# Kernel tuning notes

Measured on AMD Instinct MI355X. Metric: run time of the kernel, lower is better.

The kernel has to match this reference:

```python
import jax, jax.numpy as jnp
import numpy as np

BATCH, NUM_BSS, NUM_USERS, M, N = 32, 8, 32, 128, 4
LAGR_ITERS = 8
PSEUDOINV_SVAL_THRESH = 1e-12


def herm(a):
    return 0.5 * (a + jnp.swapaxes(a, -1, -2).conj())


def setup_inputs() -> dict:
    key = jax.random.key(0)
    ks = jax.random.split(key, 7)
    v_re = jax.random.normal(ks[0], (BATCH, NUM_USERS, M, N), jnp.float32)
    v_im = jax.random.normal(ks[1], (BATCH, NUM_USERS, M, N), jnp.float32)
    H_re = jax.random.normal(ks[2], (NUM_BSS, NUM_USERS, N, M), jnp.float32)
    H_im = jax.random.normal(ks[3], (NUM_BSS, NUM_USERS, N, M), jnp.float32)
    noise_pow = jax.random.uniform(ks[4], (BATCH, NUM_USERS), jnp.float32, 0.05, 1.0)
    rweights = jax.random.uniform(ks[5], (BATCH, NUM_USERS), jnp.float32, 0.1, 1.0)
    bss_pow = jnp.ones((BATCH, NUM_BSS), jnp.float32)
    assign = jax.random.randint(ks[6], (NUM_USERS,), 0, NUM_BSS).astype(jnp.int32)
    return {"v_re": v_re, "v_im": v_im, "H_re": H_re, "H_im": H_im,
            "noise_pow": noise_pow, "rweights": rweights, "bss_pow": bss_pow,
            "assign": assign}


def reference(v_re, v_im, H_re, H_im, noise_pow, rweights, bss_pow, assign):
    V = v_re + 1j * v_im          # [B,K,M,N] precoders
    H = H_re + 1j * H_im          # [C,K,N,M] channel BS c -> user k
    K = V.shape[1]
    C = H.shape[0]
    Ndim = V.shape[-1]
    eyeN = jnp.eye(Ndim, dtype=V.dtype)

    # Hg[j, i] = channel from assigned-BS-of-user-j to user i
    Hg = H[assign]                                    # [K,K,N,M]
    # downlink covariance per user i: noise*I + sum_j (H[bs_j,i] V_j)(.)^H
    HV = jnp.einsum('jinm,bjmp->bijnp', Hg, V)        # [B,Ki,Kj,N,N]
    cov = jnp.einsum('bijnp,bijqp->binq', HV, HV.conj())
    cov = herm(cov + noise_pow[..., None, None] * eyeN)
    icov = herm(jnp.linalg.inv(cov))                  # [B,K,N,N]

    idx = jnp.arange(K)
    Hd = Hg[idx, idx]                                 # [K,N,M] direct channels
    HdV = jnp.einsum('knm,bkmp->bknp', Hd, V)         # [B,K,N,N]
    u = jnp.einsum('bknq,bkqp->bknp', icov, HdV)      # receive filters
    w_inv = herm(eyeN - jnp.einsum('bkqn,bkqp->bknp', u.conj(), HdV))
    w = herm(jnp.linalg.inv(w_inv))                   # MSE weights (w_poly=None)
    uwu = herm(jnp.einsum('bknp,bkpq,bkrq->bknr', u, w, u.conj()))
    # v_tilde = H_ii^H u w * rate_weight
    vt = jnp.einsum('knm,bknp,bkpq->bkmq', Hd.conj(), u, w) * rweights[..., None, None]

    # uplink covariance per BS c: sum_k rw_k * H[c,k]^H uwu_k H[c,k]
    ul = herm(jnp.einsum('cknm,bkno,ckop,bk->bcmp', H.conj(), uwu, H, rweights))

    # aux per BS: sum over assigned users of v_tilde v_tilde^H
    Q = jnp.einsum('bkmn,bkpn->bkmp', vt, vt.conj())  # [B,K,M,M]
    aux = jnp.moveaxis(
        jax.ops.segment_sum(jnp.moveaxis(Q, 1, 0), assign, num_segments=C), 0, 1)  # [B,C,M,M]

    lam, E = jnp.linalg.eigh(ul)                      # [B,C,M], [B,C,M,M]
    lam = jnp.maximum(lam, 0.0)
    c = jnp.maximum(jnp.einsum('bcmi,bcmp,bcpi->bci', E.conj(), aux, E).real, 0.0)
    c = c / bss_pow[..., None]

    # solve sum_i c_i/(lam_i+mu)^2 = 1 for mu >= 0 by bisection in [0, sqrt(sum c)]
    hi = jnp.sqrt(jnp.sum(c, -1))
    lo = jnp.zeros_like(hi)
    for _ in range(LAGR_ITERS):
        mid = 0.5 * (lo + hi)
        f = jnp.sum(c / jnp.square(lam + mid[..., None] + 1e-20), -1)
        gt = f > 1.0
        lo = jnp.where(gt, mid, lo)
        hi = jnp.where(gt, hi, mid)
    mu = jnp.maximum(0.5 * (lo + hi), 0.0)            # [B,C]

    # pseudo-inverse of loaded UL covariance via its eigendecomposition
    lam_l = lam + mu[..., None]
    lam_l = jnp.where(lam_l < PSEUDOINV_SVAL_THRESH, 1e12, lam_l)
    inv_aug = herm(jnp.einsum('bcmi,bci,bcni->bcmn', E, 1.0 / lam_l, E.conj()))

    # v update: v_k = inv_aug[assign_k] @ v_tilde_k
    v_out = jnp.einsum('bkmp,bkpn->bkmn', inv_aug[:, assign], vt)  # [B,K,M,N]
    return v_out
```

## Files before the change

kernel.cpp:

```cpp
#include <hip/hip_runtime.h>

#define B_ 32
#define C_ 8
#define K_ 32

__device__ __forceinline__ float2 cmul(float2 a, float2 b) {
  return make_float2(a.x*b.x - a.y*b.y, a.x*b.y + a.y*b.x);
}
__device__ __forceinline__ float2 cmulc(float2 a, float2 b) {
  return make_float2(a.x*b.x + a.y*b.y, a.y*b.x - a.x*b.y);
}
__device__ __forceinline__ float2 cadd(float2 a, float2 b){ return make_float2(a.x+b.x, a.y+b.y); }
__device__ __forceinline__ float2 csub(float2 a, float2 b){ return make_float2(a.x-b.x, a.y-b.y); }
__device__ __forceinline__ int SK(int r){ return r + ((r >> 3) << 1); }

__device__ void herm4_inv(float2 a[4][4], float2 out[4][4]) {
  float idg[4];
  for (int j = 0; j < 4; ++j) {
    float d = sqrtf(fmaxf(a[j][j].x, 1e-30f));
    float id = 1.f / d;
    idg[j] = id;
    a[j][j] = make_float2(d, 0.f);
    for (int r = j+1; r < 4; ++r) { a[r][j].x *= id; a[r][j].y *= id; }
    for (int c = j+1; c < 4; ++c)
      for (int r = c; r < 4; ++r)
        a[r][c] = csub(a[r][c], cmulc(a[r][j], a[c][j]));
  }
  float2 li[4][4];
  for (int j = 0; j < 4; ++j) {
    li[j][j] = make_float2(idg[j], 0.f);
    for (int r = j+1; r < 4; ++r) {
      float2 s = make_float2(0.f, 0.f);
      for (int d = j; d < r; ++d) s = cadd(s, cmul(a[r][d], li[d][j]));
      li[r][j] = make_float2(-s.x*idg[r], -s.y*idg[r]);
    }
  }
  for (int p = 0; p < 4; ++p)
    for (int q = 0; q < 4; ++q) {
      float2 s = make_float2(0.f, 0.f);
      for (int d = (p > q ? p : q); d < 4; ++d)
        s = cadd(s, cmulc(li[d][q], li[d][p]));
      out[p][q] = s;
    }
}

__global__ __launch_bounds__(512, 2) void k_fused(
    const float* __restrict__ v_re, const float* __restrict__ v_im,
    const float* __restrict__ H_re, const float* __restrict__ H_im,
    const float* __restrict__ noise_pow, const float* __restrict__ rweights,
    const float* __restrict__ bss_pow, const int* __restrict__ assign_g,
    void* __restrict__ outp, int omode)
{
  const int t = threadIdx.x;
  const int lane = t & 63, wid = t >> 6;
  const int blk = blockIdx.x;
  const int b = blk >> 3, c = blk & 7;
  const int tm = t >> 4, tp = t & 15;
  const int rbase = tm * 4, cbase = tp * 8;

  __shared__ __align__(16) float2 Arena[4160];
  __shared__ __align__(16) float2 pS[1024];
  __shared__ __align__(16) float2 dBS2[256];
  __shared__ __align__(16) float2 vS[128];
  __shared__ __align__(16) float2 wS[160];
  __shared__ __align__(16) float2 colS[160];
  __shared__ __align__(16) float2 pvS[128];
  __shared__ __align__(16) float2 tauS[128];
  __shared__ float dS[128], eS[128], cpS[128];
  __shared__ float red[8];
  __shared__ int asg[K_], ulist[K_], nc_s;

  float2* Wall = pS;
  float2* uwS  = pS + 512;
  float2* Vs   = Arena;
  float2* Tb   = Arena + 776;
  float2* covS = Arena + 1288;
  float2* HdVS = Arena + 1800;
  float2* Hs   = Arena;
  float2* Ys   = Arena + 520;
  float2* Pd   = Arena;
  float2* Bs   = Arena;

  if (t < K_) asg[t] = assign_g[t];
  if (t == 0) {
    int n2 = 0;
    for (int k = 0; k < K_; ++k) if (assign_g[k] == c) ulist[n2++] = k;
    nc_s = n2;
  }
  {
    const int k = t >> 4, n = (t >> 2) & 3, q = t & 3;
    covS[t] = make_float2((n == q) ? noise_pow[b*K_ + k] : 0.f, 0.f);
  }
  __syncthreads();
  const int nc = nc_s;
  if (nc == 0) return;
  const int cols = 4 * nc;
  const int qmax = (cols + 15) >> 4;
  const int passes = (cols + 31) >> 5;

  {
    const int pn = t >> 2;
    const int qt = t & 3;
    const int kk = pn >> 2, nn = pn & 3;
    const float2* Vq = Vs + qt*2;
    for (int j = 0; j < K_; ++j) {
      const int vb = (b*K_ + j) * 512;
      Vs[(t >> 2)*6 + (t & 3) + (t >> 7)*2] = make_float2(v_re[vb + t], v_im[vb + t]);
      __syncthreads();
      const int hb = ((asg[j]*K_ + kk)*4 + nn) * 128;
      float2 a0 = {0,0}, a1 = {0,0}, a2 = {0,0}, a3 = {0,0};
      for (int m4 = qt*32; m4 < qt*32 + 32; m4 += 4) {
        const float4 hre = *(const float4*)&H_re[hb + m4];
        const float4 him = *(const float4*)&H_im[hb + m4];
        const float hx[4] = {hre.x, hre.y, hre.z, hre.w};
        const float hy[4] = {him.x, him.y, him.z, him.w};
        #pragma unroll
        for (int i = 0; i < 4; ++i) {
          const float4 v01 = *(const float4*)&Vq[(m4 + i)*6];
          const float4 v23 = *(const float4*)&Vq[(m4 + i)*6 + 2];
          a0.x += hx[i]*v01.x - hy[i]*v01.y; a0.y += hx[i]*v01.y + hy[i]*v01.x;
          a1.x += hx[i]*v01.z - hy[i]*v01.w; a1.y += hx[i]*v01.w + hy[i]*v01.z;
          a2.x += hx[i]*v23.x - hy[i]*v23.y; a2.y += hx[i]*v23.y + hy[i]*v23.x;
          a3.x += hx[i]*v23.z - hy[i]*v23.w; a3.y += hx[i]*v23.w + hy[i]*v23.z;
        }
      }
      #pragma unroll
      for (int o = 1; o <= 2; o <<= 1) {
        a0.x += __shfl_xor(a0.x, o, 64); a0.y += __shfl_xor(a0.y, o, 64);
        a1.x += __shfl_xor(a1.x, o, 64); a1.y += __shfl_xor(a1.y, o, 64);
        a2.x += __shfl_xor(a2.x, o, 64); a2.y += __shfl_xor(a2.y, o, 64);
        a3.x += __shfl_xor(a3.x, o, 64); a3.y += __shfl_xor(a3.y, o, 64);
      }
      if (qt == 0) {
        Tb[pn*4 + 0] = a0; Tb[pn*4 + 1] = a1; Tb[pn*4 + 2] = a2; Tb[pn*4 + 3] = a3;
      }
      __syncthreads();
      {
        const int k2 = t >> 4, n2 = (t >> 2) & 3, q2 = t & 3;
        float2 acc = covS[t];
        #pragma unroll
        for (int p = 0; p < 4; ++p)
          acc = cadd(acc, cmulc(Tb[(k2*4 + n2)*4 + p], Tb[(k2*4 + q2)*4 + p]));
        covS[t] = acc;
        if (k2 == j) HdVS[k2*16 + n2*4 + q2] = Tb[(k2*4 + n2)*4 + q2];
      }
      __syncthreads();
    }
  }

  if (t < K_) {
    const int k = t;
    float2 a[4][4], ic[4][4], hv[4][4], u[4][4], wi[4][4], w[4][4], uw[4][4], W[4][4];
    const float rwk = rweights[b*K_ + k];
    for (int r = 0; r < 4; ++r)
      for (int c2 = 0; c2 < 4; ++c2) a[r][c2] = covS[k*16 + r*4 + c2];
    herm4_inv(a, ic);
    for (int r = 0; r < 4; ++r)
      for (int c2 = 0; c2 < 4; ++c2) hv[r][c2] = HdVS[k*16 + r*4 + c2];
    for (int n = 0; n < 4; ++n)
      for (int p = 0; p < 4; ++p) {
        float2 s = {0,0};
        for (int q = 0; q < 4; ++q) s = cadd(s, cmul(ic[n][q], hv[q][p]));
        u[n][p] = s;
      }
    for (int n = 0; n < 4; ++n)
      for (int p = 0; p < 4; ++p) {
        float2 s = make_float2((n == p) ? 1.f : 0.f, 0.f);
        for (int q = 0; q < 4; ++q) s = csub(s, cmulc(hv[q][p], u[q][n]));
        wi[n][p] = s;
      }
    herm4_inv(wi, w);
    for (int n = 0; n < 4; ++n)
      for (int q = 0; q < 4; ++q) {
        float2 s = {0,0};
        for (int p = 0; p < 4; ++p) s = cadd(s, cmul(u[n][p], w[p][q]));
        uw[n][q] = s;
      }
    for (int n = 0; n < 4; ++n)
      for (int r = 0; r < 4; ++r) {
        float2 s = {0,0};
        for (int q = 0; q < 4; ++q) s = cadd(s, cmulc(uw[n][q], u[r][q]));
        W[n][r] = make_float2(s.x * rwk, s.y * rwk);
      }
    for (int n = 0; n < 4; ++n)
      for (int r = n; r < 4; ++r) {
        float2 x1 = W[n][r], x2 = W[r][n];
        float2 hm = make_float2(0.5f*(x1.x + x2.x), 0.5f*(x1.y - x2.y));
        W[n][r] = hm; W[r][n] = make_float2(hm.x, -hm.y);
      }
    for (int idx = 0; idx < 16; ++idx) {
      uwS[k*16 + idx]  = uw[idx >> 2][idx & 3];
      Wall[k*16 + idx] = W[idx >> 2][idx & 3];
    }
  }
  __syncthreads();

  float2 Bv[4][8];
  #pragma unroll
  for (int j = 0; j < 4; ++j)
    #pragma unroll
    for (int q = 0; q < 8; ++q) Bv[j][q] = make_float2(0.f, 0.f);
  float trp = 0.f;
  #pragma unroll
  for (int q = 0; q < 8; ++q) {
    const int col = tp + 16*q;
    const int slot = col >> 2, qn = col & 3;
    if (slot < nc) {
      const int k = ulist[slot];
      const float rwk = rweights[b*K_ + k];
      const int hb = (c*K_ + k) * 512;
      float2 acc0 = {0,0}, acc1 = {0,0}, acc2 = {0,0}, acc3 = {0,0};
      #pragma unroll
      for (int n = 0; n < 4; ++n) {
        const float2 uwv = uwS[k*16 + n*4 + qn];
        const float4 hre = *(const float4*)&H_re[hb + n*128 + rbase];
        const float4 him = *(const float4*)&H_im[hb + n*128 + rbase];
        acc0 = cadd(acc0, cmulc(uwv, make_float2(hre.x, him.x)));
        acc1 = cadd(acc1, cmulc(uwv, make_float2(hre.y, him.y)));
        acc2 = cadd(acc2, cmulc(uwv, make_float2(hre.z, him.z)));
        acc3 = cadd(acc3, cmulc(uwv, make_float2(hre.w, him.w)));
      }
      acc0.x *= rwk; acc0.y *= rwk; acc1.x *= rwk; acc1.y *= rwk;
      acc2.x *= rwk; acc2.y *= rwk; acc3.x *= rwk; acc3.y *= rwk;
      Bv[0][q] = acc0; Bv[1][q] = acc1; Bv[2][q] = acc2; Bv[3][q] = acc3;
      trp += acc0.x*acc0.x + acc0.y*acc0.y + acc1.x*acc1.x + acc1.y*acc1.y
           + acc2.x*acc2.x + acc2.y*acc2.y + acc3.x*acc3.x + acc3.y*acc3.y;
    }
  }
  #pragma unroll
  for (int o = 32; o >= 1; o >>= 1) trp += __shfl_xor(trp, o, 64);
  if (lane == 0) red[wid] = trp;
  __syncthreads();
  const float inv_bss = 1.f / bss_pow[b*C_ + c];
  float hi = sqrtf((red[0] + red[1] + red[2] + red[3] +
                    red[4] + red[5] + red[6] + red[7]) * inv_bss);
  float lo = 0.f;

  float2 Areg[4][8];
  #pragma unroll
  for (int j = 0; j < 4; ++j)
    #pragma unroll
    for (int cc = 0; cc < 8; ++cc) Areg[j][cc] = make_float2(0.f, 0.f);
  __syncthreads();
  for (int k = 0; k < K_; ++k) {
    const int hb = (c*K_ + k) * 512;
    Hs[(t >> 7)*130 + (t & 127)] = make_float2(H_re[hb + t], H_im[hb + t]);
    __syncthreads();
    {
      const int n = t >> 7, p = t & 127;
      float2 y = {0,0};
      #pragma unroll
      for (int o = 0; o < 4; ++o) y = cadd(y, cmul(Wall[k*16 + n*4 + o], Hs[o*130 + p]));
      Ys[n*160 + p + ((p >> 3) << 1)] = y;
    }
    __syncthreads();
    #pragma unroll
    for (int n = 0; n < 4; ++n) {
      float2 h[4], y[8];
      {
        const float4 ha = *(const float4*)&Hs[n*130 + rbase];
        const float4 hc = *(const float4*)&Hs[n*130 + rbase + 2];
        h[0] = make_float2(ha.x, ha.y); h[1] = make_float2(ha.z, ha.w);
        h[2] = make_float2(hc.x, hc.y); h[3] = make_float2(hc.z, hc.w);
        const float2* yb = &Ys[n*160 + tp*10];
        #pragma unroll
        for (int a2 = 0; a2 < 8; a2 += 2) {
          const float4 y4 = *(const float4*)&yb[a2];
          y[a2] = make_float2(y4.x, y4.y); y[a2+1] = make_float2(y4.z, y4.w);
        }
      }
      #pragma unroll
      for (int j = 0; j < 4; ++j)
        #pragma unroll
        for (int cc = 0; cc < 8; ++cc) {
          Areg[j][cc].x += h[j].x*y[cc].x + h[j].y*y[cc].y;
          Areg[j][cc].y += h[j].x*y[cc].y - h[j].y*y[cc].x;
        }
    }
    __syncthreads();
  }

  if (tp == 0) {
    #pragma unroll
    for (int j = 0; j < 4; ++j) colS[SK(rbase + j)] = Areg[j][0];
  }
  __syncthreads();

  #pragma unroll 1
  for (int i = 0; i < 127; ++i) {
    float2 vr[4], vc[8], tau, sc;
    {
      const float2 x0 = colS[SK(lane)], x1 = colS[SK(lane + 64)];
      float sig = 0.f;
      if (lane >= i + 2)      sig += x0.x*x0.x + x0.y*x0.y;
      if (lane + 64 >= i + 2) sig += x1.x*x1.x + x1.y*x1.y;
      #pragma unroll
      for (int o = 32; o >= 1; o >>= 1) sig += __shfl_xor(sig, o, 64);
      const float2 al = colS[SK(i + 1)];
      float beta;
      if (sig <= 1e-30f && fabsf(al.y) <= 1e-30f) {
        beta = al.x; tau = make_float2(0.f, 0.f); sc = make_float2(0.f, 0.f);
      } else {
        const float mag = sqrtf(al.x*al.x + al.y*al.y + sig);
        beta = (al.x >= 0.f) ? -mag : mag;
        const float ib = 1.f / beta;
        tau = make_float2((beta - al.x) * ib, -al.y * ib);
        const float dx = al.x - beta, dy = al.y;
        const float dn = 1.f / (dx*dx + dy*dy);
        sc = make_float2(dx*dn, -dy*dn);
      }
      if (t == 0) { eS[i] = beta; tauS[i] = tau; }
      #pragma unroll
      for (int j = 0; j < 4; ++j) {
        const int r = rbase + j;
        const float2 x = colS[SK(r)];
        vr[j] = (r <= i) ? make_float2(0.f, 0.f)
              : (r == i + 1 ? make_float2(1.f, 0.f) : cmul(x, sc));
      }
      {
        const int cb = SK(cbase);
        const float4 c01 = *(const float4*)&colS[cb];
        const float4 c23 = *(const float4*)&colS[cb + 2];
        const float4 c45 = *(const float4*)&colS[cb + 4];
        const float4 c67 = *(const float4*)&colS[cb + 6];
        const float2 cx[8] = { make_float2(c01.x,c01.y), make_float2(c01.z,c01.w),
                               make_float2(c23.x,c23.y), make_float2(c23.z,c23.w),
                               make_float2(c45.x,c45.y), make_float2(c45.z,c45.w),
                               make_float2(c67.x,c67.y), make_float2(c67.z,c67.w) };
        #pragma unroll
        for (int cc = 0; cc < 8; ++cc) {
          const int r = cbase + cc;
          vc[cc] = (r <= i) ? make_float2(0.f, 0.f)
                 : (r == i + 1 ? make_float2(1.f, 0.f) : cmul(cx[cc], sc));
        }
      }
    }
    {
      float2 part[4];
      #pragma unroll
      for (int j = 0; j < 4; ++j) {
        float2 s = cmul(Areg[j][0], vc[0]);
        #pragma unroll
        for (int cc = 1; cc < 8; ++cc) s = cadd(s, cmul(Areg[j][cc], vc[cc]));
        part[j] = s;
      }
      #pragma unroll
      for (int o = 1; o <= 8; o <<= 1) {
        #pragma unroll
        for (int j = 0; j < 4; ++j) {
          part[j].x += __shfl_xor(part[j].x, o, 64);
          part[j].y += __shfl_xor(part[j].y, o, 64);
        }
      }
      #pragma unroll
      for (int j = 0; j < 4; ++j) if (tp == j) pvS[rbase + j] = part[j];
      #pragma unroll
      for (int q = 0; q < 8; ++q) {
        if (q >= qmax) continue;
        float2 s = {0.f, 0.f};
        #pragma unroll
        for (int j = 0; j < 4; ++j) s = cadd(s, cmulc(Bv[j][q], vr[j]));
        Pd[tm*130 + tp + 16*q] = s;
      }
    }
    __syncthreads();

    if (wid == 0) {
      float2 p0 = {0.f,0.f}, p1 = {0.f,0.f};
      if (lane > i)      p0 = cmul(tau, pvS[lane]);
      if (lane + 64 > i) p1 = cmul(tau, pvS[lane + 64]);
      float2 v0, v1;
      v0 = (lane <= i) ? make_float2(0.f,0.f)
         : (lane == i + 1 ? make_float2(1.f,0.f) : cmul(colS[SK(lane)], sc));
      { const int r1 = lane + 64;
        v1 = (r1 <= i) ? make_float2(0.f,0.f)
           : (r1 == i + 1 ? make_float2(1.f,0.f) : cmul(colS[SK(r1)], sc)); }
      float2 d0 = cadd(cmulc(p0, v0), cmulc(p1, v1));
      #pragma unroll
      for (int o = 32; o >= 1; o >>= 1) {
        d0.x += __shfl_xor(d0.x, o, 64);
        d0.y += __shfl_xor(d0.y, o, 64);
      }
      const float alr = -0.5f * (tau.x*d0.x + tau.y*d0.y);
      wS[SK(lane)]      = cadd(p0, make_float2(alr*v0.x, alr*v0.y));
      wS[SK(lane + 64)] = cadd(p1, make_float2(alr*v1.x, alr*v1.y));
    } else if (t < 320) {
      const int col = (t - 64) & 127;
      const int half = (t - 64) >> 7;
      float2 s = {0.f, 0.f};
      #pragma unroll
      for (int g = 0; g < 16; ++g) s = cadd(s, Pd[(half*16 + g)*130 + col]);
      dBS2[half*128 + col] = s;
    }
    __syncthreads();

    {
      float2 wr[4], wc[8];
      #pragma unroll
      for (int j = 0; j < 4; ++j) wr[j] = wS[SK(rbase + j)];
      {
        const int cb = SK(cbase);
        const float4 w01 = *(const float4*)&wS[cb];
        const float4 w23 = *(const float4*)&wS[cb + 2];
        const float4 w45 = *(const float4*)&wS[cb + 4];
        const float4 w67 = *(const float4*)&wS[cb + 6];
        wc[0] = make_float2(w01.x,w01.y); wc[1] = make_float2(w01.z,w01.w);
        wc[2] = make_float2(w23.x,w23.y); wc[3] = make_float2(w23.z,w23.w);
        wc[4] = make_float2(w45.x,w45.y); wc[5] = make_float2(w45.z,w45.w);
        wc[6] = make_float2(w67.x,w67.y); wc[7] = make_float2(w67.z,w67.w);
      }
      #pragma unroll
      for (int j = 0; j < 4; ++j)
        #pragma unroll
        for (int cc = 0; cc < 8; ++cc)
          Areg[j][cc] = csub(Areg[j][cc], cadd(cmulc(vr[j], wc[cc]), cmulc(wr[j], vc[cc])));
      const float2 tauc = make_float2(tau.x, -tau.y);
      #pragma unroll
      for (int q = 0; q < 8; ++q) {
        if (q >= qmax) continue;
        const float2 dBt = cmul(tauc, cadd(dBS2[tp + 16*q], dBS2[128 + tp + 16*q]));
        #pragma unroll
        for (int j = 0; j < 4; ++j) Bv[j][q] = csub(Bv[j][q], cmul(dBt, vr[j]));
      }
      if (tp == (i >> 3)) {
        #pragma unroll
        for (int cc = 0; cc < 8; ++cc) if (cc == (i & 7)) {
          #pragma unroll
          for (int j = 0; j < 4; ++j) if (rbase + j >= i + 1) Areg[j][cc] = vr[j];
        }
      }
      if (tp == ((i + 1) >> 3)) {
        #pragma unroll
        for (int cc = 0; cc < 8; ++cc) if (cc == ((i + 1) & 7)) {
          #pragma unroll
          for (int j = 0; j < 4; ++j) colS[SK(rbase + j)] = Areg[j][cc];
        }
      }
    }
    __syncthreads();
  }

  if (tp == (tm >> 1)) {
    const int co = (tm & 1) * 4;
    #pragma unroll
    for (int j = 0; j < 4; ++j)
      #pragma unroll
      for (int cc = 0; cc < 8; ++cc)
        if (cc == co + j) dS[rbase + j] = Areg[j][cc].x;
  }
  __syncthreads();

  for (int it = 0; it <= 8; ++it) {
    const float mu = 0.5f * (lo + hi);
    float fsum = 0.f;
    #pragma unroll
    for (int p = 0; p < 4; ++p) {
      if (p >= passes) continue;
      __syncthreads();
      #pragma unroll
      for (int j = 0; j < 4; ++j) {
        Bs[(rbase + j)*32 + tp]      = Bv[j][2*p];
        Bs[(rbase + j)*32 + tp + 16] = Bv[j][2*p + 1];
      }
      __syncthreads();
      if (wid == 0) {
        const int colg = 32*p + lane;
        const bool act = (lane < 32) && (colg < cols);
        float m = dS[0] + mu;
        float im = 1.f / m;
        float2 g = act ? Bs[lane] : make_float2(0.f, 0.f);
        g.x *= im; g.y *= im;
        if (act) Bs[lane] = g;
        float cp = eS[0] * im;
        if (lane == 0) cpS[0] = cp;
        for (int r = 1; r < 128; ++r) {
          const float e0 = eS[r-1];
          m = dS[r] + mu - e0 * cp;
          im = 1.f / m;
          float2 gr = act ? Bs[r*32 + lane] : make_float2(0.f, 0.f);
          gr.x = (gr.x - e0 * g.x) * im;
          gr.y = (gr.y - e0 * g.y) * im;
          g = gr;
          if (act) Bs[r*32 + lane] = gr;
          if (r < 127) { cp = eS[r] * im; if (lane == 0) cpS[r] = cp; }
        }
        float2 z = g;
        float acc = z.x*z.x + z.y*z.y;
        for (int r = 126; r >= 0; --r) {
          const float cpr = cpS[r];
          const float2 gp = act ? Bs[r*32 + lane] : make_float2(0.f, 0.f);
          z.x = gp.x - cpr * z.x;
          z.y = gp.y - cpr * z.y;
          acc += z.x*z.x + z.y*z.y;
          if (it == 8 && act) Bs[r*32 + lane] = z;
        }
        if (act) fsum += acc;
      }
      if (it == 8) {
        __syncthreads();
        #pragma unroll
        for (int j = 0; j < 4; ++j) {
          Bv[j][2*p]     = Bs[(rbase + j)*32 + tp];
          Bv[j][2*p + 1] = Bs[(rbase + j)*32 + tp + 16];
        }
      }
    }
    if (it < 8 && wid == 0) {
      #pragma unroll
      for (int o = 32; o >= 1; o >>= 1) fsum += __shfl_xor(fsum, o, 64);
      const float f = fsum * inv_bss;
      if (f > 1.0f) lo = mu; else hi = mu;
    }
  }
  __syncthreads();

  #pragma unroll 1
  for (int i = 126; i >= 0; --i) {
    if (t < 128 && t <= i) vS[t] = make_float2(0.f, 0.f);
    if (tp == (i >> 3)) {
      #pragma unroll
      for (int cc = 0; cc < 8; ++cc) if (cc == (i & 7)) {
        #pragma unroll
        for (int j = 0; j < 4; ++j) if (rbase + j >= i + 1) vS[rbase + j] = Areg[j][cc];
      }
    }
    __syncthreads();
    float2 vr[4];
    #pragma unroll
    for (int j = 0; j < 4; ++j) vr[j] = vS[rbase + j];
    #pragma unroll
    for (int q = 0; q < 8; ++q) {
      if (q >= qmax) continue;
      float2 s = {0.f, 0.f};
      #pragma unroll
      for (int j = 0; j < 4; ++j) s = cadd(s, cmulc(Bv[j][q], vr[j]));
      Pd[tm*130 + tp + 16*q] = s;
    }
    __syncthreads();
    if (t < 256) {
      const int col = t & 127;
      const int half = t >> 7;
      float2 s = {0.f, 0.f};
      #pragma unroll
      for (int g = 0; g < 16; ++g) s = cadd(s, Pd[(half*16 + g)*130 + col]);
      dBS2[half*128 + col] = s;
    }
    __syncthreads();
    {
      const float2 tau2 = tauS[i];
      #pragma unroll
      for (int q = 0; q < 8; ++q) {
        if (q >= qmax) continue;
        const float2 dBt = cmul(tau2, cadd(dBS2[tp + 16*q], dBS2[128 + tp + 16*q]));
        #pragma unroll
        for (int j = 0; j < 4; ++j) Bv[j][q] = csub(Bv[j][q], cmul(dBt, vr[j]));
      }
    }
  }

  #pragma unroll
  for (int q = 0; q < 8; ++q) {
    const int col = tp + 16*q;
    const int slot = col >> 2, qn = col & 3;
    if (slot < nc) {
      const int k = ulist[slot];
      const size_t base = (size_t)(b*K_ + k) * 512;
      #pragma unroll
      for (int j = 0; j < 4; ++j) {
        const size_t oe = base + (size_t)(rbase + j)*4 + qn;
        if (omode == 0) ((float2*)outp)[oe] = Bv[j][q];
        else            ((float*)outp)[oe]  = Bv[j][q].x;
      }
    }
  }
}

extern "C" void kernel_launch(void* const* d_in, const int* in_sizes, int n_in,
                              void* d_out, int out_size, void* d_ws, size_t ws_size,
                              hipStream_t stream)
{
  (void)in_sizes; (void)n_in; (void)d_ws; (void)ws_size;
  const float* v_re   = (const float*)d_in[0];
  const float* v_im   = (const float*)d_in[1];
  const float* H_re   = (const float*)d_in[2];
  const float* H_im   = (const float*)d_in[3];
  const float* noise  = (const float*)d_in[4];
  const float* rw     = (const float*)d_in[5];
  const float* bss    = (const float*)d_in[6];
  const int*   assign = (const int*)d_in[7];

  const int omode = (out_size == B_*K_*128*4) ? 1 : 0;

  hipLaunchKernelGGL(k_fused, dim3(B_*C_), dim3(512), 0, stream,
                     v_re, v_im, H_re, H_im, noise, rw, bss, assign, d_out, omode);
}
```

Baseline: 1.337 ms.

## Double block size to 1024 threads, halve rows per thread, process two users per sync

Doubles the workgroup to 1024 threads, so each thread owns 2 rows of the 128x128 matrix instead of 4. That halves the register tile for the Householder tridiagonalisation and the back-transformation. The covariance and UL-matrix accumulation stages now handle two users per barrier round. Partial sums are reduced with cross-lane shuffles before going to shared memory. The aim is more parallelism in the serial 127-step reduction loops, at the cost of more threads contending at each barrier and possibly lower occupancy per CU.

Result: slower. 3.112 ms (+132.8%).

```diff
diff --git a/kernel.cpp b/kernel.cpp
--- a/kernel.cpp
+++ b/kernel.cpp
@@ -44,7 +44,7 @@
     }
 }
 
-__global__ __launch_bounds__(512, 2) void k_fused(
+__global__ __launch_bounds__(1024, 4) void k_fused(
     const float* __restrict__ v_re, const float* __restrict__ v_im,
     const float* __restrict__ H_re, const float* __restrict__ H_im,
     const float* __restrict__ noise_pow, const float* __restrict__ rweights,
@@ -56,7 +56,7 @@
   const int blk = blockIdx.x;
   const int b = blk >> 3, c = blk & 7;
   const int tm = t >> 4, tp = t & 15;
-  const int rbase = tm * 4, cbase = tp * 8;
+  const int rbase = tm * 2, cbase = tp * 8;
 
   __shared__ __align__(16) float2 Arena[4160];
   __shared__ __align__(16) float2 pS[1024];
@@ -67,17 +67,13 @@
   __shared__ __align__(16) float2 pvS[128];
   __shared__ __align__(16) float2 tauS[128];
   __shared__ float dS[128], eS[128], cpS[128];
-  __shared__ float red[8];
+  __shared__ float red[16];
   __shared__ int asg[K_], ulist[K_], nc_s;
 
   float2* Wall = pS;
   float2* uwS  = pS + 512;
-  float2* Vs   = Arena;
-  float2* Tb   = Arena + 776;
-  float2* covS = Arena + 1288;
-  float2* HdVS = Arena + 1800;
-  float2* Hs   = Arena;
-  float2* Ys   = Arena + 520;
+  float2* covS = Arena + 2576;
+  float2* HdVS = Arena + 3088;
   float2* Pd   = Arena;
   float2* Bs   = Arena;
 
@@ -87,7 +83,7 @@
     for (int k = 0; k < K_; ++k) if (assign_g[k] == c) ulist[n2++] = k;
     nc_s = n2;
   }
-  {
+  if (t < 512) {
     const int k = t >> 4, n = (t >> 2) & 3, q = t & 3;
     covS[t] = make_float2((n == q) ? noise_pow[b*K_ + k] : 0.f, 0.f);
   }
@@ -99,50 +95,68 @@
   const int passes = (cols + 31) >> 5;
 
   {
-    const int pn = t >> 2;
-    const int qt = t & 3;
+    const int pn = t >> 3, qt = t & 7;
     const int kk = pn >> 2, nn = pn & 3;
-    const float2* Vq = Vs + qt*2;
-    for (int j = 0; j < K_; ++j) {
-      const int vb = (b*K_ + j) * 512;
-      Vs[(t >> 2)*6 + (t & 3) + (t >> 7)*2] = make_float2(v_re[vb + t], v_im[vb + t]);
-      __syncthreads();
-      const int hb = ((asg[j]*K_ + kk)*4 + nn) * 128;
-      float2 a0 = {0,0}, a1 = {0,0}, a2 = {0,0}, a3 = {0,0};
-      for (int m4 = qt*32; m4 < qt*32 + 32; m4 += 4) {
-        const float4 hre = *(const float4*)&H_re[hb + m4];
-        const float4 him = *(const float4*)&H_im[hb + m4];
-        const float hx[4] = {hre.x, hre.y, hre.z, hre.w};
-        const float hy[4] = {him.x, him.y, him.z, him.w};
-        #pragma unroll
-        for (int i = 0; i < 4; ++i) {
-          const float4 v01 = *(const float4*)&Vq[(m4 + i)*6];
-          const float4 v23 = *(const float4*)&Vq[(m4 + i)*6 + 2];
-          a0.x += hx[i]*v01.x - hy[i]*v01.y; a0.y += hx[i]*v01.y + hy[i]*v01.x;
-          a1.x += hx[i]*v01.z - hy[i]*v01.w; a1.y += hx[i]*v01.w + hy[i]*v01.z;
-          a2.x += hx[i]*v23.x - hy[i]*v23.y; a2.y += hx[i]*v23.y + hy[i]*v23.x;
-          a3.x += hx[i]*v23.z - hy[i]*v23.w; a3.y += hx[i]*v23.w + hy[i]*v23.z;
-        }
-      }
-      #pragma unroll
-      for (int o = 1; o <= 2; o <<= 1) {
-        a0.x += __shfl_xor(a0.x, o, 64); a0.y += __shfl_xor(a0.y, o, 64);
-        a1.x += __shfl_xor(a1.x, o, 64); a1.y += __shfl_xor(a1.y, o, 64);
-        a2.x += __shfl_xor(a2.x, o, 64); a2.y += __shfl_xor(a2.y, o, 64);
-        a3.x += __shfl_xor(a3.x, o, 64); a3.y += __shfl_xor(a3.y, o, 64);
+    const int sb = (qt >> 1) << 1;
+    const int sA = t & 511, bfA = t >> 9;
+    for (int j = 0; j < K_; j += 2) {
+      { const int vb = (b*K_ + j + bfA) * 512;
+        Arena[bfA*776 + (sA >> 2)*6 + (sA & 3) + (sA >> 7)*2] =
+            make_float2(v_re[vb + sA], v_im[vb + sA]); }
+      __syncthreads();
+      float2 rr[2][4];
+      #pragma unroll
+      for (int bf = 0; bf < 2; ++bf) {
+        const float2* Vq = Arena + bf*776 + sb;
+        const int hb = ((asg[j + bf]*K_ + kk)*4 + nn) * 128;
+        float2 a0 = {0,0}, a1 = {0,0}, a2 = {0,0}, a3 = {0,0};
+        for (int m4 = qt*16; m4 < qt*16 + 16; m4 += 4) {
+          const float4 hre = *(const float4*)&H_re[hb + m4];
+          const float4 him = *(const float4*)&H_im[hb + m4];
+          const float hx[4] = {hre.x, hre.y, hre.z, hre.w};
+          const float hy[4] = {him.x, him.y, him.z, him.w};
+          #pragma unroll
+          for (int i2 = 0; i2 < 4; ++i2) {
+            const float4 v01 = *(const float4*)&Vq[(m4 + i2)*6];
+            const float4 v23 = *(const float4*)&Vq[(m4 + i2)*6 + 2];
+            a0.x += hx[i2]*v01.x - hy[i2]*v01.y; a0.y += hx[i2]*v01.y + hy[i2]*v01.x;
+            a1.x += hx[i2]*v01.z - hy[i2]*v01.w; a1.y += hx[i2]*v01.w + hy[i2]*v01.z;
+            a2.x += hx[i2]*v23.x - hy[i2]*v23.y; a2.y += hx[i2]*v23.y + hy[i2]*v23.x;
+            a3.x += hx[i2]*v23.z - hy[i2]*v23.w; a3.y += hx[i2]*v23.w + hy[i2]*v23.z;
+          }
+        }
+        rr[bf][0] = a0; rr[bf][1] = a1; rr[bf][2] = a2; rr[bf][3] = a3;
+      }
+      #pragma unroll
+      for (int o = 1; o <= 4; o <<= 1) {
+        #pragma unroll
+        for (int bf = 0; bf < 2; ++bf)
+          #pragma unroll
+          for (int p = 0; p < 4; ++p) {
+            rr[bf][p].x += __shfl_xor(rr[bf][p].x, o, 64);
+            rr[bf][p].y += __shfl_xor(rr[bf][p].y, o, 64);
+          }
       }
       if (qt == 0) {
-        Tb[pn*4 + 0] = a0; Tb[pn*4 + 1] = a1; Tb[pn*4 + 2] = a2; Tb[pn*4 + 3] = a3;
-      }
-      __syncthreads();
-      {
+        #pragma unroll
+        for (int p = 0; p < 4; ++p) {
+          Arena[1552 + pn*4 + p] = rr[0][p];
+          Arena[2064 + pn*4 + p] = rr[1][p];
+        }
+      }
+      __syncthreads();
+      if (t < 512) {
         const int k2 = t >> 4, n2 = (t >> 2) & 3, q2 = t & 3;
         float2 acc = covS[t];
         #pragma unroll
         for (int p = 0; p < 4; ++p)
-          acc = cadd(acc, cmulc(Tb[(k2*4 + n2)*4 + p], Tb[(k2*4 + q2)*4 + p]));
+          acc = cadd(acc, cmulc(Arena[1552 + (k2*4 + n2)*4 + p], Arena[1552 + (k2*4 + q2)*4 + p]));
+        #pragma unroll
+        for (int p = 0; p < 4; ++p)
+          acc = cadd(acc, cmulc(Arena[2064 + (k2*4 + n2)*4 + p], Arena[2064 + (k2*4 + q2)*4 + p]));
         covS[t] = acc;
-        if (k2 == j) HdVS[k2*16 + n2*4 + q2] = Tb[(k2*4 + n2)*4 + q2];
+        if (k2 == j)     HdVS[k2*16 + n2*4 + q2] = Arena[1552 + (k2*4 + n2)*4 + q2];
+        if (k2 == j + 1) HdVS[k2*16 + n2*4 + q2] = Arena[2064 + (k2*4 + n2)*4 + q2];
       }
       __syncthreads();
     }
@@ -195,9 +209,9 @@
   }
   __syncthreads();
 
-  float2 Bv[4][8];
+  float2 Bv[2][8];
   #pragma unroll
-  for (int j = 0; j < 4; ++j)
+  for (int j = 0; j < 2; ++j)
     #pragma unroll
     for (int q = 0; q < 8; ++q) Bv[j][q] = make_float2(0.f, 0.f);
   float trp = 0.f;
@@ -209,22 +223,18 @@
       const int k = ulist[slot];
       const float rwk = rweights[b*K_ + k];
       const int hb = (c*K_ + k) * 512;
-      float2 acc0 = {0,0}, acc1 = {0,0}, acc2 = {0,0}, acc3 = {0,0};
+      float2 acc0 = {0,0}, acc1 = {0,0};
       #pragma unroll
       for (int n = 0; n < 4; ++n) {
         const float2 uwv = uwS[k*16 + n*4 + qn];
-        const float4 hre = *(const float4*)&H_re[hb + n*128 + rbase];
-        const float4 him = *(const float4*)&H_im[hb + n*128 + rbase];
+        const float2 hre = *(const float2*)&H_re[hb + n*128 + rbase];
+        const float2 him = *(const float2*)&H_im[hb + n*128 + rbase];
         acc0 = cadd(acc0, cmulc(uwv, make_float2(hre.x, him.x)));
         acc1 = cadd(acc1, cmulc(uwv, make_float2(hre.y, him.y)));
-        acc2 = cadd(acc2, cmulc(uwv, make_float2(hre.z, him.z)));
-        acc3 = cadd(acc3, cmulc(uwv, make_float2(hre.w, him.w)));
       }
       acc0.x *= rwk; acc0.y *= rwk; acc1.x *= rwk; acc1.y *= rwk;
-      acc2.x *= rwk; acc2.y *= rwk; acc3.x *= rwk; acc3.y *= rwk;
-      Bv[0][q] = acc0; Bv[1][q] = acc1; Bv[2][q] = acc2; Bv[3][q] = acc3;
-      trp += acc0.x*acc0.x + acc0.y*acc0.y + acc1.x*acc1.x + acc1.y*acc1.y
-           + acc2.x*acc2.x + acc2.y*acc2.y + acc3.x*acc3.x + acc3.y*acc3.y;
+      Bv[0][q] = acc0; Bv[1][q] = acc1;
+      trp += acc0.x*acc0.x + acc0.y*acc0.y + acc1.x*acc1.x + acc1.y*acc1.y;
     }
   }
   #pragma unroll
@@ -232,63 +242,66 @@
   if (lane == 0) red[wid] = trp;
   __syncthreads();
   const float inv_bss = 1.f / bss_pow[b*C_ + c];
-  float hi = sqrtf((red[0] + red[1] + red[2] + red[3] +
-                    red[4] + red[5] + red[6] + red[7]) * inv_bss);
+  float rs = 0.f;
+  #pragma unroll
+  for (int w2 = 0; w2 < 16; ++w2) rs += red[w2];
+  float hi = sqrtf(rs * inv_bss);
   float lo = 0.f;
 
-  float2 Areg[4][8];
+  float2 Areg[2][8];
   #pragma unroll
-  for (int j = 0; j < 4; ++j)
+  for (int j = 0; j < 2; ++j)
     #pragma unroll
     for (int cc = 0; cc < 8; ++cc) Areg[j][cc] = make_float2(0.f, 0.f);
-  __syncthreads();
-  for (int k = 0; k < K_; ++k) {
-    const int hb = (c*K_ + k) * 512;
-    Hs[(t >> 7)*130 + (t & 127)] = make_float2(H_re[hb + t], H_im[hb + t]);
-    __syncthreads();
-    {
-      const int n = t >> 7, p = t & 127;
-      float2 y = {0,0};
-      #pragma unroll
-      for (int o = 0; o < 4; ++o) y = cadd(y, cmul(Wall[k*16 + n*4 + o], Hs[o*130 + p]));
-      Ys[n*160 + p + ((p >> 3) << 1)] = y;
-    }
-    __syncthreads();
-    #pragma unroll
-    for (int n = 0; n < 4; ++n) {
-      float2 h[4], y[8];
-      {
-        const float4 ha = *(const float4*)&Hs[n*130 + rbase];
-        const float4 hc = *(const float4*)&Hs[n*130 + rbase + 2];
-        h[0] = make_float2(ha.x, ha.y); h[1] = make_float2(ha.z, ha.w);
-        h[2] = make_float2(hc.x, hc.y); h[3] = make_float2(hc.z, hc.w);
-        const float2* yb = &Ys[n*160 + tp*10];
-        #pragma unroll
-        for (int a2 = 0; a2 < 8; a2 += 2) {
-          const float4 y4 = *(const float4*)&yb[a2];
-          y[a2] = make_float2(y4.x, y4.y); y[a2+1] = make_float2(y4.z, y4.w);
-        }
-      }
-      #pragma unroll
-      for (int j = 0; j < 4; ++j)
-        #pragma unroll
-        for (int cc = 0; cc < 8; ++cc) {
-          Areg[j][cc].x += h[j].x*y[cc].x + h[j].y*y[cc].y;
-          Areg[j][cc].y += h[j].x*y[cc].y - h[j].y*y[cc].x;
-        }
-    }
-    __syncthreads();
-  }
-
-  if (tp == 0) {
-    #pragma unroll
-    for (int j = 0; j < 4; ++j) colS[SK(rbase + j)] = Areg[j][0];
-  }
+  {
+    const int sA = t & 511, bfA = t >> 9;
+    for (int k = 0; k < K_; k += 2) {
+      { const int hb = (c*K_ + k + bfA) * 512;
+        Arena[bfA*520 + (sA >> 7)*130 + (sA & 127)] =
+            make_float2(H_re[hb + sA], H_im[hb + sA]); }
+      __syncthreads();
+      { const int n = sA >> 7, p = sA & 127;
+        const float2* HsB = Arena + bfA*520;
+        const int kb = (k + bfA)*16 + n*4;
+        float2 y = {0,0};
+        #pragma unroll
+        for (int o = 0; o < 4; ++o) y = cadd(y, cmul(Wall[kb + o], HsB[o*130 + p]));
+        Arena[1040 + bfA*640 + n*160 + p + ((p >> 3) << 1)] = y; }
+      __syncthreads();
+      #pragma unroll
+      for (int bf = 0; bf < 2; ++bf) {
+        const float2* HsB = Arena + bf*520;
+        const float2* YsB = Arena + 1040 + bf*640;
+        #pragma unroll
+        for (int n = 0; n < 4; ++n) {
+          const float4 ha = *(const float4*)&HsB[n*130 + rbase];
+          const float2 h0 = make_float2(ha.x, ha.y), h1 = make_float2(ha.z, ha.w);
+          const float2* yb = &YsB[n*160 + tp*10];
+          float2 y[8];
+          #pragma unroll
+          for (int a2 = 0; a2 < 8; a2 += 2) {
+            const float4 y4 = *(const float4*)&yb[a2];
+            y[a2] = make_float2(y4.x, y4.y); y[a2+1] = make_float2(y4.z, y4.w);
+          }
+          #pragma unroll
+          for (int cc = 0; cc < 8; ++cc) {
+            Areg[0][cc].x += h0.x*y[cc].x + h0.y*y[cc].y;
+            Areg[0][cc].y += h0.x*y[cc].y - h0.y*y[cc].x;
+            Areg[1][cc].x += h1.x*y[cc].x + h1.y*y[cc].y;
+            Areg[1][cc].y += h1.x*y[cc].y - h1.y*y[cc].x;
+          }
+        }
+      }
+      __syncthreads();
+    }
+  }
+
+  if (tp == 0) { colS[SK(rbase)] = Areg[0][0]; colS[SK(rbase + 1)] = Areg[1][0]; }
   __syncthreads();
 
   #pragma unroll 1
   for (int i = 0; i < 127; ++i) {
-    float2 vr[4], vc[8], tau, sc;
+    float2 vr[2], vc[8], tau, sc;
     {
       const float2 x0 = colS[SK(lane)], x1 = colS[SK(lane + 64)];
       float sig = 0.f;
@@ -311,7 +324,7 @@
       }
       if (t == 0) { eS[i] = beta; tauS[i] = tau; }
       #pragma unroll
-      for (int j = 0; j < 4; ++j) {
+      for (int j = 0; j < 2; ++j) {
         const int r = rbase + j;
         const float2 x = colS[SK(r)];
         vr[j] = (r <= i) ? make_float2(0.f, 0.f)
@@ -336,9 +349,9 @@
       }
     }
     {
-      float2 part[4];
-      #pragma unroll
-      for (int j = 0; j < 4; ++j) {
+      float2 part[2];
+      #pragma unroll
+      for (int j = 0; j < 2; ++j) {
         float2 s = cmul(Areg[j][0], vc[0]);
         #pragma unroll
         for (int cc = 1; cc < 8; ++cc) s = cadd(s, cmul(Areg[j][cc], vc[cc]));
@@ -347,20 +360,20 @@
       #pragma unroll
       for (int o = 1; o <= 8; o <<= 1) {
         #pragma unroll
-        for (int j = 0; j < 4; ++j) {
+        for (int j = 0; j < 2; ++j) {
           part[j].x += __shfl_xor(part[j].x, o, 64);
           part[j].y += __shfl_xor(part[j].y, o, 64);
         }
       }
-      #pragma unroll
-      for (int j = 0; j < 4; ++j) if (tp == j) pvS[rbase + j] = part[j];
+      if (tp == 0) pvS[rbase]     = part[0];
+      if (tp == 1) pvS[rbase + 1] = part[1];
       #pragma unroll
       for (int q = 0; q < 8; ++q) {
         if (q >= qmax) continue;
-        float2 s = {0.f, 0.f};
-        #pragma unroll
-        for (int j = 0; j < 4; ++j) s = cadd(s, cmulc(Bv[j][q], vr[j]));
-        Pd[tm*130 + tp + 16*q] = s;
+        float2 s = cadd(cmulc(Bv[0][q], vr[0]), cmulc(Bv[1][q], vr[1]));
+        s.x += __shfl_xor(s.x, 16, 64); s.y += __shfl_xor(s.y, 16, 64);
+        s.x += __shfl_xor(s.x, 32, 64); s.y += __shfl_xor(s.y, 32, 64);
+        if (lane < 16) Pd[wid*128 + tp + 16*q] = s;
       }
     }
     __syncthreads();
@@ -389,15 +402,14 @@
       const int half = (t - 64) >> 7;
       float2 s = {0.f, 0.f};
       #pragma unroll
-      for (int g = 0; g < 16; ++g) s = cadd(s, Pd[(half*16 + g)*130 + col]);
+      for (int g = 0; g < 8; ++g) s = cadd(s, Pd[(half*8 + g)*128 + col]);
       dBS2[half*128 + col] = s;
     }
     __syncthreads();
 
     {
-      float2 wr[4], wc[8];
-      #pragma unroll
-      for (int j = 0; j < 4; ++j) wr[j] = wS[SK(rbase + j)];
+      float2 wr[2], wc[8];
+      wr[0] = wS[SK(rbase)]; wr[1] = wS[SK(rbase + 1)];
       {
         const int cb = SK(cbase);
         const float4 w01 = *(const float4*)&wS[cb];
@@ -410,7 +422,7 @@
         wc[6] = make_float2(w67.x,w67.y); wc[7] = make_float2(w67.z,w67.w);
       }
       #pragma unroll
-      for (int j = 0; j < 4; ++j)
+      for (int j = 0; j < 2; ++j)
         #pragma unroll
         for (int cc = 0; cc < 8; ++cc)
           Areg[j][cc] = csub(Areg[j][cc], cadd(cmulc(vr[j], wc[cc]), cmulc(wr[j], vc[cc])));
@@ -420,33 +432,33 @@
         if (q >= qmax) continue;
         const float2 dBt = cmul(tauc, cadd(dBS2[tp + 16*q], dBS2[128 + tp + 16*q]));
         #pragma unroll
-        for (int j = 0; j < 4; ++j) Bv[j][q] = csub(Bv[j][q], cmul(dBt, vr[j]));
+        for (int j = 0; j < 2; ++j) Bv[j][q] = csub(Bv[j][q], cmul(dBt, vr[j]));
       }
       if (tp == (i >> 3)) {
         #pragma unroll
         for (int cc = 0; cc < 8; ++cc) if (cc == (i & 7)) {
           #pragma unroll
-          for (int j = 0; j < 4; ++j) if (rbase + j >= i + 1) Areg[j][cc] = vr[j];
+          for (int j = 0; j < 2; ++j) if (rbase + j >= i + 1) Areg[j][cc] = vr[j];
         }
       }
       if (tp == ((i + 1) >> 3)) {
         #pragma unroll
         for (int cc = 0; cc < 8; ++cc) if (cc == ((i + 1) & 7)) {
           #pragma unroll
-          for (int j = 0; j < 4; ++j) colS[SK(rbase + j)] = Areg[j][cc];
+          for (int j = 0; j < 2; ++j) colS[SK(rbase + j)] = Areg[j][cc];
         }
       }
     }
     __syncthreads();
   }
 
-  if (tp == (tm >> 1)) {
-    const int co = (tm & 1) * 4;
-    #pragma unroll
-    for (int j = 0; j < 4; ++j)
-      #pragma unroll
-      for (int cc = 0; cc < 8; ++cc)
-        if (cc == co + j) dS[rbase + j] = Areg[j][cc].x;
+  #pragma unroll
+  for (int j = 0; j < 2; ++j) {
+    const int r = rbase + j;
+    if (tp == (r >> 3)) {
+      #pragma unroll
+      for (int cc = 0; cc < 8; ++cc) if (cc == (r & 7)) dS[r] = Areg[j][cc].x;
+    }
   }
   __syncthreads();
 
@@ -458,7 +470,7 @@
       if (p >= passes) continue;
       __syncthreads();
       #pragma unroll
-      for (int j = 0; j < 4; ++j) {
+      for (int j = 0; j < 2; ++j) {
         Bs[(rbase + j)*32 + tp]      = Bv[j][2*p];
         Bs[(rbase + j)*32 + tp + 16] = Bv[j][2*p + 1];
       }
@@ -499,7 +511,7 @@
       if (it == 8) {
         __syncthreads();
         #pragma unroll
-        for (int j = 0; j < 4; ++j) {
+        for (int j = 0; j < 2; ++j) {
           Bv[j][2*p]     = Bs[(rbase + j)*32 + tp];
           Bv[j][2*p + 1] = Bs[(rbase + j)*32 + tp + 16];
         }
@@ -521,20 +533,19 @@
       #pragma unroll
       for (int cc = 0; cc < 8; ++cc) if (cc == (i & 7)) {
         #pragma unroll
-        for (int j = 0; j < 4; ++j) if (rbase + j >= i + 1) vS[rbase + j] = Areg[j][cc];
+        for (int j = 0; j < 2; ++j) if (rbase + j >= i + 1) vS[rbase + j] = Areg[j][cc];
       }
     }
     __syncthreads();
-    float2 vr[4];
-    #pragma unroll
-    for (int j = 0; j < 4; ++j) vr[j] = vS[rbase + j];
+    float2 vr2[2];
+    vr2[0] = vS[rbase]; vr2[1] = vS[rbase + 1];
     #pragma unroll
     for (int q = 0; q < 8; ++q) {
       if (q >= qmax) continue;
-      float2 s = {0.f, 0.f};
-      #pragma unroll
-      for (int j = 0; j < 4; ++j) s = cadd(s, cmulc(Bv[j][q], vr[j]));
-      Pd[tm*130 + tp + 16*q] = s;
+      float2 s = cadd(cmulc(Bv[0][q], vr2[0]), cmulc(Bv[1][q], vr2[1]));
+      s.x += __shfl_xor(s.x, 16, 64); s.y += __shfl_xor(s.y, 16, 64);
+      s.x += __shfl_xor(s.x, 32, 64); s.y += __shfl_xor(s.y, 32, 64);
+      if (lane < 16) Pd[wid*128 + tp + 16*q] = s;
     }
     __syncthreads();
     if (t < 256) {
@@ -542,7 +553,7 @@
       const int half = t >> 7;
       float2 s = {0.f, 0.f};
       #pragma unroll
-      for (int g = 0; g < 16; ++g) s = cadd(s, Pd[(half*16 + g)*130 + col]);
+      for (int g = 0; g < 8; ++g) s = cadd(s, Pd[(half*8 + g)*128 + col]);
       dBS2[half*128 + col] = s;
     }
     __syncthreads();
@@ -553,7 +564,7 @@
         if (q >= qmax) continue;
         const float2 dBt = cmul(tau2, cadd(dBS2[tp + 16*q], dBS2[128 + tp + 16*q]));
         #pragma unroll
-        for (int j = 0; j < 4; ++j) Bv[j][q] = csub(Bv[j][q], cmul(dBt, vr[j]));
+        for (int j = 0; j < 2; ++j) Bv[j][q] = csub(Bv[j][q], cmul(dBt, vr2[j]));
       }
     }
   }
@@ -566,7 +577,7 @@
       const int k = ulist[slot];
       const size_t base = (size_t)(b*K_ + k) * 512;
       #pragma unroll
-      for (int j = 0; j < 4; ++j) {
+      for (int j = 0; j < 2; ++j) {
         const size_t oe = base + (size_t)(rbase + j)*4 + qn;
         if (omode == 0) ((float2*)outp)[oe] = Bv[j][q];
         else            ((float*)outp)[oe]  = Bv[j][q].x;
@@ -591,6 +602,6 @@
 
   const int omode = (out_size == B_*K_*128*4) ? 1 : 0;
 
-  hipLaunchKernelGGL(k_fused, dim3(B_*C_), dim3(512), 0, stream,
+  hipLaunchKernelGGL(k_fused, dim3(B_*C_), dim3(1024), 0, stream,
                      v_re, v_im, H_re, H_im, noise, rw, bss, assign, d_out, omode);
 }
```
